# Optimization experiments

Hardware: AMD Instinct MI355X
Metric: run time of the kernel (lower is better)

The kernel has to match this reference:

```python
import jax, jax.numpy as jnp
import numpy as np

B, T, E, H, C = 64, 512, 768, 128, 18


def setup_inputs() -> dict:
    key = jax.random.key(0)
    ks = jax.random.split(key, 16)
    s = 1.0 / np.sqrt(H)
    inp = {
        "x": jax.random.normal(ks[0], (B, T, E), jnp.float32),
        "attention_mask": jnp.ones((B, T), jnp.int32),
        "labels": jax.random.randint(ks[1], (B, T), 0, C, jnp.int32),
        "Wih_f": jax.random.uniform(ks[2], (4 * H, E), jnp.float32, -s, s),
        "Whh_f": jax.random.uniform(ks[3], (4 * H, H), jnp.float32, -s, s),
        "b_f": jax.random.uniform(ks[4], (4 * H,), jnp.float32, -s, s),
        "Wih_b": jax.random.uniform(ks[5], (4 * H, E), jnp.float32, -s, s),
        "Whh_b": jax.random.uniform(ks[6], (4 * H, H), jnp.float32, -s, s),
        "b_b": jax.random.uniform(ks[7], (4 * H,), jnp.float32, -s, s),
        "Wfc": jax.random.uniform(ks[8], (C, 2 * H), jnp.float32, -s, s),
        "bfc": jax.random.uniform(ks[9], (C,), jnp.float32, -s, s),
        "start_trans": jax.random.normal(ks[10], (C,), jnp.float32) * 0.1,
        "end_trans": jax.random.normal(ks[11], (C,), jnp.float32) * 0.1,
        "trans": jax.random.normal(ks[12], (C, C), jnp.float32) * 0.1,
    }
    return inp


def _lstm_dir(x, Wih, Whh, b, reverse=False):
    # x: [B, T, E] -> hidden states [B, T, H]; torch LSTM gate order i,f,g,o
    if reverse:
        x = x[:, ::-1]
    pre = jnp.einsum("bte,ge->btg", x, Wih) + b  # [B, T, 4H] input projection once
    h0 = jnp.zeros((x.shape[0], H), x.dtype)

    def step(carry, pt):
        h, c = carry
        g = pt + h @ Whh.T
        i, f, gg, o = jnp.split(g, 4, axis=-1)
        c = jax.nn.sigmoid(f) * c + jax.nn.sigmoid(i) * jnp.tanh(gg)
        h = jax.nn.sigmoid(o) * jnp.tanh(c)
        return (h, c), h

    _, hs = jax.lax.scan(step, (h0, h0), jnp.swapaxes(pre, 0, 1))
    hs = jnp.swapaxes(hs, 0, 1)
    if reverse:
        hs = hs[:, ::-1]
    return hs


def _crf_loglik(em, tags, mask, start, end, trans):
    # pytorch-crf log-likelihood, batch_first. em [B,T,C], tags/mask [B,T]
    b, t, _ = em.shape
    maskf = mask.astype(em.dtype)
    tags = tags.astype(jnp.int32)
    # numerator: score of the given tag path
    em_sc = jnp.take_along_axis(em, tags[..., None], axis=2)[..., 0]  # [B,T]
    num = start[tags[:, 0]] + em_sc[:, 0]
    num = num + jnp.sum(em_sc[:, 1:] * maskf[:, 1:], axis=1)
    num = num + jnp.sum(trans[tags[:, :-1], tags[:, 1:]] * maskf[:, 1:], axis=1)
    last_idx = jnp.sum(mask.astype(jnp.int32), axis=1) - 1
    last_tags = jnp.take_along_axis(tags, last_idx[:, None], axis=1)[:, 0]
    num = num + end[last_tags]
    # denominator: forward algorithm (logsumexp recurrence over time)
    alpha0 = start + em[:, 0]  # [B,C]

    def step(alpha, inp):
        e_t, m_t = inp
        new = jax.scipy.special.logsumexp(alpha[:, :, None] + trans[None], axis=1) + e_t
        return jnp.where(m_t[:, None], new, alpha), None

    alpha, _ = jax.lax.scan(
        step, alpha0,
        (jnp.swapaxes(em[:, 1:], 0, 1), jnp.swapaxes(mask[:, 1:].astype(bool), 0, 1)),
    )
    den = jax.scipy.special.logsumexp(alpha + end, axis=1)
    return num - den


def _viterbi(em, start, end, trans):
    # em [B,T,C] -> best path [B,T] (full mask)
    s0 = start + em[:, 0]

    def fstep(score, e_t):
        cand = score[:, :, None] + trans[None]  # [B,C,C]
        return jnp.max(cand, axis=1) + e_t, jnp.argmax(cand, axis=1)

    score, bptr = jax.lax.scan(fstep, s0, jnp.swapaxes(em[:, 1:], 0, 1))  # bptr [T-1,B,C]
    last = jnp.argmax(score + end, axis=1)  # [B]

    def bstep(tag, ptr_t):
        prev = jnp.take_along_axis(ptr_t, tag[:, None], axis=1)[:, 0]
        return prev, prev

    _, path = jax.lax.scan(bstep, last, bptr, reverse=True)  # [T-1,B]
    return jnp.concatenate([jnp.swapaxes(path, 0, 1), last[:, None]], axis=1)


def reference(x, attention_mask, labels, Wih_f, Whh_f, b_f, Wih_b, Whh_b, b_b,
              Wfc, bfc, start_trans, end_trans, trans):
    hf = _lstm_dir(x, Wih_f, Whh_f, b_f, reverse=False)
    hb = _lstm_dir(x, Wih_b, Whh_b, b_b, reverse=True)
    seq = jnp.concatenate([hf, hb], axis=-1)  # [B,T,2H]
    em = seq @ Wfc.T + bfc  # [B,T,C] emissions
    mask = attention_mask.astype(bool)
    llh = _crf_loglik(em, labels, mask, start_trans, end_trans, trans)
    loss = -jnp.sum(llh) / x.shape[0]  # reduction='sum' then / batch_size
    path = _viterbi(em, start_trans, end_trans, trans) + 1  # res_paths = x+1
    return path, loss
```

## Files before the change

### kernel.cpp

```cpp
#include <hip/hip_runtime.h>
#include <hip/hip_bf16.h>
#include <math.h>

typedef __attribute__((ext_vector_type(8))) short short8;
typedef __attribute__((ext_vector_type(4))) float f32x4;

constexpr int nB = 64, nT = 512, nE = 768, nH = 128, nG = 512, nC = 18;
constexpr int nBT = nB * nT;

__device__ __forceinline__ float bf2f(unsigned short u) { return __uint_as_float(((unsigned int)u) << 16); }
__device__ __forceinline__ unsigned short f2bf(float f) {
  __hip_bfloat16 h = __float2bfloat16(f);
  return *reinterpret_cast<unsigned short*>(&h);
}
__device__ __forceinline__ float rlane(float v, int lane) {
  return __uint_as_float(__builtin_amdgcn_readlane(__float_as_uint(v), lane));
}
__device__ __forceinline__ float fast_sig(float x) {
  return __builtin_amdgcn_rcpf(1.0f + __builtin_amdgcn_exp2f(-1.44269504f * x));
}
__device__ __forceinline__ float fast_tanh(float x) {
  return 1.0f - 2.0f * __builtin_amdgcn_rcpf(1.0f + __builtin_amdgcn_exp2f(2.88539008f * x));
}
__device__ __forceinline__ float fast_exp(float x) { return __builtin_amdgcn_exp2f(1.44269504f * x); }
__device__ __forceinline__ float fast_log(float x) { return __builtin_amdgcn_logf(x) * 0.69314718f; }

__global__ __launch_bounds__(256) void cvt_kernel(const float* __restrict__ in,
                                                  unsigned short* __restrict__ out, int n8) {
  int i = blockIdx.x * blockDim.x + threadIdx.x;
  const int stride = gridDim.x * blockDim.x;
  for (; i < n8; i += stride) {
    const float4 a = ((const float4*)in)[(size_t)i * 2];
    const float4 b = ((const float4*)in)[(size_t)i * 2 + 1];
    unsigned short u[8] = {f2bf(a.x), f2bf(a.y), f2bf(a.z), f2bf(a.w),
                           f2bf(b.x), f2bf(b.y), f2bf(b.z), f2bf(b.w)};
    ((float4*)out)[i] = *(float4*)u;
  }
}

__global__ __launch_bounds__(256) void proj_kernel(
    const float* __restrict__ x,
    const unsigned short* __restrict__ wfb, const unsigned short* __restrict__ wbb,
    const float* __restrict__ biasF, const float* __restrict__ biasB,
    unsigned short* __restrict__ Pf, unsigned short* __restrict__ Pb)
{
  const int bid = blockIdx.x;
  const int mt = bid & 255, sub = bid >> 8;
  const int dir = sub >> 2, nt = sub & 3;
  const unsigned short* W = dir ? wbb : wfb;
  const float* bias = dir ? biasB : biasF;
  unsigned short* P = dir ? Pb : Pf;
  const int m0 = mt * 128, n0 = nt * 128;

  __shared__ unsigned short As[128 * 40];
  __shared__ unsigned short Bs[128 * 40];
  const int tid = threadIdx.x;
  const int w = tid >> 6, lane = tid & 63, l15 = lane & 15, l4 = lane >> 4;
  const int wr = w >> 1, wc = w & 1;
  const int srow = tid >> 1, shalf = tid & 1;

  const float* srcA = x + (size_t)(m0 + srow) * nE + shalf * 16;
  const unsigned short* srcB = W + (size_t)(n0 + srow) * nE + shalf * 16;

  f32x4 acc[4][4];
#pragma unroll
  for (int i = 0; i < 4; ++i)
#pragma unroll
    for (int j = 0; j < 4; ++j) acc[i][j] = (f32x4){0.f, 0.f, 0.f, 0.f};

  for (int k0 = 0; k0 < nE; k0 += 32) {
    const float4 a0 = *(const float4*)(srcA + k0);
    const float4 a1 = *(const float4*)(srcA + k0 + 4);
    const float4 a2 = *(const float4*)(srcA + k0 + 8);
    const float4 a3 = *(const float4*)(srcA + k0 + 12);
    const float4 b0 = *(const float4*)(srcB + k0);
    const float4 b1 = *(const float4*)(srcB + k0 + 8);
    unsigned short ua[16] = {f2bf(a0.x), f2bf(a0.y), f2bf(a0.z), f2bf(a0.w),
                             f2bf(a1.x), f2bf(a1.y), f2bf(a1.z), f2bf(a1.w),
                             f2bf(a2.x), f2bf(a2.y), f2bf(a2.z), f2bf(a2.w),
                             f2bf(a3.x), f2bf(a3.y), f2bf(a3.z), f2bf(a3.w)};
    __syncthreads();
    *(float4*)&As[srow * 40 + shalf * 16] = *(float4*)&ua[0];
    *(float4*)&As[srow * 40 + shalf * 16 + 8] = *(float4*)&ua[8];
    *(float4*)&Bs[srow * 40 + shalf * 16] = b0;
    *(float4*)&Bs[srow * 40 + shalf * 16 + 8] = b1;
    __syncthreads();
    short8 af[4], bfr[4];
#pragma unroll
    for (int i = 0; i < 4; ++i) af[i] = *(const short8*)&As[(wr * 64 + i * 16 + l15) * 40 + l4 * 8];
#pragma unroll
    for (int j = 0; j < 4; ++j) bfr[j] = *(const short8*)&Bs[(wc * 64 + j * 16 + l15) * 40 + l4 * 8];
#pragma unroll
    for (int i = 0; i < 4; ++i)
#pragma unroll
      for (int j = 0; j < 4; ++j)
        acc[i][j] = __builtin_amdgcn_mfma_f32_16x16x32_bf16(af[i], bfr[j], acc[i][j], 0, 0, 0);
  }
  float bv[4];
#pragma unroll
  for (int j = 0; j < 4; ++j) bv[j] = bias[n0 + wc * 64 + j * 16 + l15];
#pragma unroll
  for (int i = 0; i < 4; ++i) {
#pragma unroll
    for (int j = 0; j < 4; ++j) {
      const int col = n0 + wc * 64 + j * 16 + l15;
#pragma unroll
      for (int r = 0; r < 4; ++r) {
        const int row = m0 + wr * 64 + i * 16 + l4 * 4 + r;
        P[(size_t)row * nG + col] = f2bf(acc[i][j][r] + bv[j]);
      }
    }
  }
}

__global__ __launch_bounds__(512, 1) void lstm_kernel(
    const unsigned short* __restrict__ Pf, const unsigned short* __restrict__ Pb,
    const float* __restrict__ WhhF, const float* __restrict__ WhhB,
    unsigned short* __restrict__ hf, unsigned short* __restrict__ hb)
{
  const int bid = blockIdx.x;
  const int dir = bid & 1, grp = bid >> 1;
  const int b0 = grp * 4;
  const unsigned short* pre = dir ? Pb : Pf;
  const float* Whh = dir ? WhhB : WhhF;
  unsigned short* hout = dir ? hb : hf;

  const int tid = threadIdx.x, w = tid >> 6, lane = tid & 63;
  const int l15 = lane & 15, l4 = lane >> 4;
  const int batch = l15 & 3, msel = l15 >> 2;
  const int cell = w * 16 + msel * 4 + l4;
  const int swz = batch * 40;

  __shared__ unsigned short h_lds[2 * 4 * 128];

  short8 Af[4][4];
#pragma unroll
  for (int m = 0; m < 4; ++m) {
    const int gp = w * 64 + m * 16 + l15;
    const int gorig = (gp & 3) * 128 + (gp >> 2);
#pragma unroll
    for (int kk = 0; kk < 4; ++kk) {
      const float* wp = Whh + (size_t)gorig * nH + kk * 32 + l4 * 8;
      const float4 v0 = *(const float4*)wp;
      const float4 v1 = *(const float4*)(wp + 4);
      unsigned short u[8] = {f2bf(v0.x), f2bf(v0.y), f2bf(v0.z), f2bf(v0.w),
                             f2bf(v1.x), f2bf(v1.y), f2bf(v1.z), f2bf(v1.w)};
      Af[m][kk] = *(short8*)u;
    }
  }
  for (int i = tid; i < 2 * 4 * 128; i += 512) h_lds[i] = 0;

  float c_state = 0.f;
  const unsigned short* pbase = pre + (size_t)(b0 + batch) * nT * nG + cell;

  unsigned short pA[4], pB[4];
  {
    const int tt0 = dir ? (nT - 1) : 0;
    const int tt1 = dir ? (nT - 2) : 1;
#pragma unroll
    for (int r = 0; r < 4; ++r) pA[r] = pbase[(size_t)tt0 * nG + r * 128];
#pragma unroll
    for (int r = 0; r < 4; ++r) pB[r] = pbase[(size_t)tt1 * nG + r * 128];
  }
  __syncthreads();

#define LSTM_STEP(RB, T, BUFC)                                                   \
  {                                                                              \
    const int ttime = dir ? (nT - 1 - (T)) : (T);                                \
    float pg[4];                                                                 \
    _Pragma("unroll")                                                            \
    for (int r = 0; r < 4; ++r) pg[r] = bf2f(BUFC[r]);                           \
    {                                                                            \
      const int tl = ((T) + 2 < nT) ? (T) + 2 : (T);                             \
      const int ttl = dir ? (nT - 1 - tl) : tl;                                  \
      _Pragma("unroll")                                                          \
      for (int r = 0; r < 4; ++r) BUFC[r] = pbase[(size_t)ttl * nG + r * 128];   \
    }                                                                            \
    short8 bfr[4];                                                               \
    _Pragma("unroll")                                                            \
    for (int kk = 0; kk < 4; ++kk) {                                             \
      const int idx = (RB) * 512 + batch * 128 + ((kk * 32 + l4 * 8) ^ swz);     \
      bfr[kk] = *(const short8*)&h_lds[idx];                                     \
    }                                                                            \
    f32x4 acc[4];                                                                \
    _Pragma("unroll")                                                            \
    for (int m = 0; m < 4; ++m) acc[m] = (f32x4){0.f, 0.f, 0.f, 0.f};            \
    _Pragma("unroll")                                                            \
    for (int kk = 0; kk < 4; ++kk)                                               \
      _Pragma("unroll")                                                          \
      for (int m = 0; m < 4; ++m)                                                \
        acc[m] = __builtin_amdgcn_mfma_f32_16x16x32_bf16(Af[m][kk], bfr[kk], acc[m], 0, 0, 0); \
    const float g0 = msel < 2 ? (msel == 0 ? acc[0][0] : acc[1][0]) : (msel == 2 ? acc[2][0] : acc[3][0]); \
    const float g1 = msel < 2 ? (msel == 0 ? acc[0][1] : acc[1][1]) : (msel == 2 ? acc[2][1] : acc[3][1]); \
    const float g2 = msel < 2 ? (msel == 0 ? acc[0][2] : acc[1][2]) : (msel == 2 ? acc[2][2] : acc[3][2]); \
    const float g3 = msel < 2 ? (msel == 0 ? acc[0][3] : acc[1][3]) : (msel == 2 ? acc[2][3] : acc[3][3]); \
    const float gi = g0 + pg[0], gf = g1 + pg[1], gg = g2 + pg[2], go = g3 + pg[3]; \
    c_state = fast_sig(gf) * c_state + fast_sig(gi) * fast_tanh(gg);             \
    const float hval = fast_sig(go) * fast_tanh(c_state);                        \
    const unsigned short hu = f2bf(hval);                                        \
    h_lds[((RB) ^ 1) * 512 + batch * 128 + (cell ^ swz)] = hu;                   \
    hout[((size_t)(b0 + batch) * nT + ttime) * nH + cell] = hu;                  \
    asm volatile("s_waitcnt lgkmcnt(0)" ::: "memory");                           \
    __builtin_amdgcn_sched_barrier(0);                                           \
    __builtin_amdgcn_s_barrier();                                                \
  }

  for (int t2 = 0; t2 < nT; t2 += 2) {
    LSTM_STEP(0, t2, pA)
    LSTM_STEP(1, t2 + 1, pB)
  }
#undef LSTM_STEP
}

__global__ __launch_bounds__(256) void em_kernel(
    const unsigned short* __restrict__ hf, const unsigned short* __restrict__ hb,
    const float* __restrict__ Wfc, const float* __restrict__ bfc,
    float* __restrict__ em)
{
  __shared__ float seq[32][260];
  __shared__ float Wf[18][260];
  const int tid = threadIdx.x;
  const int row0 = blockIdx.x * 32;
  for (int i = tid; i < 32 * 32; i += 256) {
    const int r = i >> 5, seg = i & 31;
    const unsigned short* src = (seg < 16) ? (hf + (size_t)(row0 + r) * nH + seg * 8)
                                           : (hb + (size_t)(row0 + r) * nH + (seg - 16) * 8);
    const float4 v = *(const float4*)src;
    const unsigned short* u = (const unsigned short*)&v;
#pragma unroll
    for (int k = 0; k < 8; ++k) seq[r][seg * 8 + k] = bf2f(u[k]);
  }
  for (int i = tid; i < nC * 256; i += 256) {
    const int cc = i >> 8, k = i & 255;
    Wf[cc][k] = Wfc[cc * 256 + k];
  }
  __syncthreads();
  for (int o = tid; o < 32 * nC; o += 256) {
    const int r = o / nC, cc = o - r * nC;
    float acc = bfc[cc];
    const float4* s4 = (const float4*)&seq[r][0];
    const float4* w4 = (const float4*)&Wf[cc][0];
#pragma unroll
    for (int q = 0; q < 64; ++q) {
      const float4 a = s4[q]; const float4 wv = w4[q];
      acc += a.x * wv.x + a.y * wv.y + a.z * wv.z + a.w * wv.w;
    }
    em[(size_t)(row0 + r) * nC + cc] = acc;
  }
}

__global__ __launch_bounds__(128) void crfvit_kernel(
    const float* __restrict__ em, const int* __restrict__ labels,
    const int* __restrict__ mask, const float* __restrict__ start,
    const float* __restrict__ endt, const float* __restrict__ trans,
    float* __restrict__ llh, float* __restrict__ out_path)
{
  const int b = blockIdx.x; const int tid = threadIdx.x;
  __shared__ float tr[nC * nC];
  __shared__ unsigned char bp[(nT - 1) * nC];
  __shared__ unsigned char path[nT];
  for (int i = tid; i < nC * nC; i += 128) tr[i] = trans[i];
  __syncthreads();
  const float* eb = em + (size_t)b * nT * nC;

#define MAX18(c) fmaxf(fmaxf(fmaxf(fmaxf(fmaxf(c[0], c[1]), c[2]), fmaxf(fmaxf(c[3], c[4]), c[5])),           \
                             fmaxf(fmaxf(fmaxf(c[6], c[7]), c[8]), fmaxf(fmaxf(c[9], c[10]), c[11]))),        \
                       fmaxf(fmaxf(fmaxf(c[12], c[13]), c[14]), fmaxf(fmaxf(c[15], c[16]), c[17])))

  if (tid < 64) {
    const int l = tid;
    const int lc = l < nC ? l : nC - 1;
    const int* tg = labels + (size_t)b * nT;
    const int* mk = mask + (size_t)b * nT;

    float np = 0.f; int cnt = 0;
    for (int t = l; t < nT; t += 64) {
      const int tag = tg[t];
      const float e = eb[(size_t)t * nC + tag];
      if (t == 0) np += start[tag] + e;
      else np += (float)mk[t] * (e + tr[tg[t - 1] * nC + tag]);
      cnt += mk[t];
    }
#pragma unroll
    for (int off = 32; off; off >>= 1) { np += __shfl_xor(np, off); cnt += __shfl_xor(cnt, off); }
    const float num = np + endt[tg[cnt - 1]];

    float trc[nC];
#pragma unroll
    for (int i = 0; i < nC; ++i) trc[i] = tr[i * nC + lc];

    float alpha_r = start[lc] + eb[lc];
    float eA = eb[1 * nC + lc];
    float eB = eb[2 * nC + lc];
    float eC = eb[3 * nC + lc];
    for (int tk = 0; tk < 8; ++tk) {
      const unsigned long long mb = __ballot(mk[tk * 64 + l] != 0);
      for (int tt = (tk == 0 ? 1 : 0); tt < 64; ++tt) {
        const int t = tk * 64 + tt;
        const float ecur = eA; eA = eB; eB = eC;
        const int tl = t + 3 < nT ? t + 3 : nT - 1;
        eC = eb[(size_t)tl * nC + lc];
        float cand[nC];
#pragma unroll
        for (int i = 0; i < nC; ++i) cand[i] = rlane(alpha_r, i) + trc[i];
        const float m = MAX18(cand);
        float ex[nC];
#pragma unroll
        for (int i = 0; i < nC; ++i) ex[i] = fast_exp(cand[i] - m);
        float s = 0.f;
#pragma unroll
        for (int i = 0; i < nC; ++i) s += ex[i];
        const float anew = m + fast_log(s) + ecur;
        alpha_r = ((mb >> tt) & 1) ? anew : alpha_r;
      }
    }
    const float v = (l < nC) ? (alpha_r + endt[l]) : -3.0e38f;
    float m = v;
#pragma unroll
    for (int off = 32; off; off >>= 1) m = fmaxf(m, __shfl_xor(m, off));
    float s = (l < nC) ? fast_exp(v - m) : 0.f;
#pragma unroll
    for (int off = 32; off; off >>= 1) s += __shfl_xor(s, off);
    if (l == 0) llh[b] = num - (m + fast_log(s));
  } else {
    const int l = tid - 64;
    const int lc = l < nC ? l : nC - 1;
    float trc[nC];
#pragma unroll
    for (int i = 0; i < nC; ++i) trc[i] = tr[i * nC + lc];

    float score_r = start[lc] + eb[lc];
    float eA = eb[1 * nC + lc];
    float eB = eb[2 * nC + lc];
    float eC = eb[3 * nC + lc];
    for (int t = 1; t < nT; ++t) {
      const float ecur = eA; eA = eB; eB = eC;
      const int tl = t + 3 < nT ? t + 3 : nT - 1;
      eC = eb[(size_t)tl * nC + lc];
      float cand[nC];
#pragma unroll
      for (int i = 0; i < nC; ++i) cand[i] = rlane(score_r, i) + trc[i];
      const float m = MAX18(cand);
      int sel[nC];
#pragma unroll
      for (int i = 0; i < nC; ++i) sel[i] = (cand[i] == m) ? i : 63;
      int arg = sel[0];
#pragma unroll
      for (int i = 1; i < nC; ++i) arg = min(arg, sel[i]);
      score_r = m + ecur;
      if (l < nC) bp[(t - 1) * nC + l] = (unsigned char)arg;
    }
    if (l == 0) {
      float mm = -3.0e38f; int last = 0;
      for (int i = 0; i < nC; ++i) {
        const float v = rlane(score_r, i) + endt[i];
        if (v > mm) { mm = v; last = i; }
      }
      path[nT - 1] = (unsigned char)last;
      int cur = last;
      for (int t = nT - 2; t >= 0; --t) { cur = bp[t * nC + cur]; path[t] = (unsigned char)cur; }
    }
    asm volatile("s_waitcnt lgkmcnt(0)" ::: "memory");
    __builtin_amdgcn_wave_barrier();
    for (int t = l; t < nT; t += 64) out_path[(size_t)b * nT + t] = (float)(path[t] + 1);
  }
#undef MAX18
}

__global__ __launch_bounds__(64) void loss_kernel(const float* __restrict__ llh, float* __restrict__ out)
{
  const int l = threadIdx.x;
  float v = llh[l];
#pragma unroll
  for (int off = 32; off; off >>= 1) v += __shfl_xor(v, off);
  if (l == 0) out[0] = -v / (float)nB;
}

extern "C" void kernel_launch(void* const* d_in, const int* in_sizes, int n_in,
                              void* d_out, int out_size, void* d_ws, size_t ws_size,
                              hipStream_t stream)
{
  const float* x      = (const float*)d_in[0];
  const int*   amask  = (const int*)d_in[1];
  const int*   labels = (const int*)d_in[2];
  const float* Wih_f  = (const float*)d_in[3];
  const float* Whh_f  = (const float*)d_in[4];
  const float* b_f    = (const float*)d_in[5];
  const float* Wih_b  = (const float*)d_in[6];
  const float* Whh_b  = (const float*)d_in[7];
  const float* b_b    = (const float*)d_in[8];
  const float* Wfc    = (const float*)d_in[9];
  const float* bfc    = (const float*)d_in[10];
  const float* start  = (const float*)d_in[11];
  const float* endt   = (const float*)d_in[12];
  const float* trans  = (const float*)d_in[13];

  float* out = (float*)d_out;
  float* ws = (float*)d_ws;
  unsigned short* preF = (unsigned short*)ws;
  unsigned short* preB = preF + (size_t)nBT * nG;
  unsigned short* hf   = preB + (size_t)nBT * nG;
  unsigned short* hb   = hf + (size_t)nBT * nH;
  float* em  = (float*)(hb + (size_t)nBT * nH);
  float* llh = em + (size_t)nBT * nC;
  unsigned short* wfb = (unsigned short*)(llh + 64);
  unsigned short* wbb = wfb + (size_t)nG * nE;

  cvt_kernel<<<192, 256, 0, stream>>>(Wih_f, wfb, nG * nE / 8);
  cvt_kernel<<<192, 256, 0, stream>>>(Wih_b, wbb, nG * nE / 8);
  proj_kernel<<<2048, 256, 0, stream>>>(x, wfb, wbb, b_f, b_b, preF, preB);
  lstm_kernel<<<32, 512, 0, stream>>>(preF, preB, Whh_f, Whh_b, hf, hb);
  em_kernel<<<1024, 256, 0, stream>>>(hf, hb, Wfc, bfc, em);
  crfvit_kernel<<<64, 128, 0, stream>>>(em, labels, amask, start, endt, trans, llh, out);
  loss_kernel<<<1, 64, 0, stream>>>(llh, out + nBT);
}
```

Before: 549.0 us.

## Fuse input projection and LSTM into one kernel with per-quarter flag handoff

Merges the input-projection GEMM and the recurrent LSTM into one persistent launch. The first 32 blocks run the recurrence while the remaining blocks compute projection tiles, ordered by time quarter and direction, and signal completion through atomic flags. LSTM blocks spin-wait on a quarter's flags before consuming it, so the sequential recurrence overlaps with the projection work. This relies on the LSTM blocks being co-resident with the producer blocks. It adds flag memsets and spin-wait overhead, and the projection tile is reshaped to 128x256 with 512 threads.

```diff
diff --git a/kernel.cpp b/kernel.cpp
--- a/kernel.cpp
+++ b/kernel.cpp
@@ -7,6 +7,7 @@
 
 constexpr int nB = 64, nT = 512, nE = 768, nH = 128, nG = 512, nC = 18;
 constexpr int nBT = nB * nT;
+constexpr int N_LSTM_BLK = 32, N_PROJ_BLK = 1024;
 
 __device__ __forceinline__ float bf2f(unsigned short u) { return __uint_as_float(((unsigned int)u) << 16); }
 __device__ __forceinline__ unsigned short f2bf(float f) {
@@ -38,86 +39,95 @@
   }
 }
 
-__global__ __launch_bounds__(256) void proj_kernel(
+__global__ __launch_bounds__(512, 2) void fused_kernel(
     const float* __restrict__ x,
     const unsigned short* __restrict__ wfb, const unsigned short* __restrict__ wbb,
     const float* __restrict__ biasF, const float* __restrict__ biasB,
-    unsigned short* __restrict__ Pf, unsigned short* __restrict__ Pb)
+    unsigned short* __restrict__ Pf, unsigned short* __restrict__ Pb,
+    const float* __restrict__ WhhF, const float* __restrict__ WhhB,
+    unsigned short* __restrict__ hf, unsigned short* __restrict__ hb,
+    int* __restrict__ flags)
 {
-  const int bid = blockIdx.x;
-  const int mt = bid & 255, sub = bid >> 8;
-  const int dir = sub >> 2, nt = sub & 3;
-  const unsigned short* W = dir ? wbb : wfb;
-  const float* bias = dir ? biasB : biasF;
-  unsigned short* P = dir ? Pb : Pf;
-  const int m0 = mt * 128, n0 = nt * 128;
-
-  __shared__ unsigned short As[128 * 40];
-  __shared__ unsigned short Bs[128 * 40];
+  __shared__ __align__(16) unsigned short smem[15360];
   const int tid = threadIdx.x;
-  const int w = tid >> 6, lane = tid & 63, l15 = lane & 15, l4 = lane >> 4;
-  const int wr = w >> 1, wc = w & 1;
-  const int srow = tid >> 1, shalf = tid & 1;
-
-  const float* srcA = x + (size_t)(m0 + srow) * nE + shalf * 16;
-  const unsigned short* srcB = W + (size_t)(n0 + srow) * nE + shalf * 16;
-
-  f32x4 acc[4][4];
-#pragma unroll
-  for (int i = 0; i < 4; ++i)
-#pragma unroll
-    for (int j = 0; j < 4; ++j) acc[i][j] = (f32x4){0.f, 0.f, 0.f, 0.f};
-
-  for (int k0 = 0; k0 < nE; k0 += 32) {
-    const float4 a0 = *(const float4*)(srcA + k0);
-    const float4 a1 = *(const float4*)(srcA + k0 + 4);
-    const float4 a2 = *(const float4*)(srcA + k0 + 8);
-    const float4 a3 = *(const float4*)(srcA + k0 + 12);
-    const float4 b0 = *(const float4*)(srcB + k0);
-    const float4 b1 = *(const float4*)(srcB + k0 + 8);
-    unsigned short ua[16] = {f2bf(a0.x), f2bf(a0.y), f2bf(a0.z), f2bf(a0.w),
-                             f2bf(a1.x), f2bf(a1.y), f2bf(a1.z), f2bf(a1.w),
-                             f2bf(a2.x), f2bf(a2.y), f2bf(a2.z), f2bf(a2.w),
-                             f2bf(a3.x), f2bf(a3.y), f2bf(a3.z), f2bf(a3.w)};
+
+  if (blockIdx.x >= N_LSTM_BLK) {
+    const int p = blockIdx.x - N_LSTM_BLK;
+    const int round = p >> 8;
+    const int r = p & 255;
+    const int dir = r & 1;
+    const int rem = r >> 1;
+    const int b = rem >> 1;
+    const int snt = rem & 1;
+    const int tq = dir ? (3 - round) : round;
+    const unsigned short* W = dir ? wbb : wfb;
+    const float* bias = dir ? biasB : biasF;
+    unsigned short* P = dir ? Pb : Pf;
+    const int m0 = b * nT + tq * 128;
+    const int n0 = snt * 256;
+
+    unsigned short* As = smem;
+    unsigned short* Bs = smem + 5120;
+
+    const int w = tid >> 6, lane = tid & 63, l15 = lane & 15, l4 = lane >> 4;
+    const int wr = w >> 2, wc = w & 3;
+    const int arow = tid >> 2, aq = tid & 3;
+    const int brow = tid >> 1, bh = tid & 1;
+
+    const float* srcA = x + (size_t)(m0 + arow) * nE + aq * 8;
+    const unsigned short* srcB = W + (size_t)(n0 + brow) * nE + bh * 16;
+
+    f32x4 acc[4][4];
+#pragma unroll
+    for (int i = 0; i < 4; ++i)
+#pragma unroll
+      for (int j = 0; j < 4; ++j) acc[i][j] = (f32x4){0.f, 0.f, 0.f, 0.f};
+
+    for (int k0 = 0; k0 < nE; k0 += 32) {
+      const float4 a0 = *(const float4*)(srcA + k0);
+      const float4 a1 = *(const float4*)(srcA + k0 + 4);
+      const float4 b0 = *(const float4*)(srcB + k0);
+      const float4 b1 = *(const float4*)(srcB + k0 + 8);
+      unsigned short ua[8] = {f2bf(a0.x), f2bf(a0.y), f2bf(a0.z), f2bf(a0.w),
+                              f2bf(a1.x), f2bf(a1.y), f2bf(a1.z), f2bf(a1.w)};
+      __syncthreads();
+      *(float4*)&As[arow * 40 + aq * 8] = *(float4*)ua;
+      *(float4*)&Bs[brow * 40 + bh * 16] = b0;
+      *(float4*)&Bs[brow * 40 + bh * 16 + 8] = b1;
+      __syncthreads();
+      short8 af[4], bfr[4];
+#pragma unroll
+      for (int i = 0; i < 4; ++i) af[i] = *(const short8*)&As[(wr * 64 + i * 16 + l15) * 40 + l4 * 8];
+#pragma unroll
+      for (int j = 0; j < 4; ++j) bfr[j] = *(const short8*)&Bs[(wc * 64 + j * 16 + l15) * 40 + l4 * 8];
+#pragma unroll
+      for (int i = 0; i < 4; ++i)
+#pragma unroll
+        for (int j = 0; j < 4; ++j)
+          acc[i][j] = __builtin_amdgcn_mfma_f32_16x16x32_bf16(af[i], bfr[j], acc[i][j], 0, 0, 0);
+    }
+    float bv[4];
+#pragma unroll
+    for (int j = 0; j < 4; ++j) bv[j] = bias[n0 + wc * 64 + j * 16 + l15];
+#pragma unroll
+    for (int i = 0; i < 4; ++i) {
+#pragma unroll
+      for (int j = 0; j < 4; ++j) {
+        const int col = n0 + wc * 64 + j * 16 + l15;
+#pragma unroll
+        for (int rr = 0; rr < 4; ++rr) {
+          const int row = m0 + wr * 64 + i * 16 + l4 * 4 + rr;
+          P[(size_t)row * nG + col] = f2bf(acc[i][j][rr] + bv[j]);
+        }
+      }
+    }
     __syncthreads();
-    *(float4*)&As[srow * 40 + shalf * 16] = *(float4*)&ua[0];
-    *(float4*)&As[srow * 40 + shalf * 16 + 8] = *(float4*)&ua[8];
-    *(float4*)&Bs[srow * 40 + shalf * 16] = b0;
-    *(float4*)&Bs[srow * 40 + shalf * 16 + 8] = b1;
-    __syncthreads();
-    short8 af[4], bfr[4];
-#pragma unroll
-    for (int i = 0; i < 4; ++i) af[i] = *(const short8*)&As[(wr * 64 + i * 16 + l15) * 40 + l4 * 8];
-#pragma unroll
-    for (int j = 0; j < 4; ++j) bfr[j] = *(const short8*)&Bs[(wc * 64 + j * 16 + l15) * 40 + l4 * 8];
-#pragma unroll
-    for (int i = 0; i < 4; ++i)
-#pragma unroll
-      for (int j = 0; j < 4; ++j)
-        acc[i][j] = __builtin_amdgcn_mfma_f32_16x16x32_bf16(af[i], bfr[j], acc[i][j], 0, 0, 0);
-  }
-  float bv[4];
-#pragma unroll
-  for (int j = 0; j < 4; ++j) bv[j] = bias[n0 + wc * 64 + j * 16 + l15];
-#pragma unroll
-  for (int i = 0; i < 4; ++i) {
-#pragma unroll
-    for (int j = 0; j < 4; ++j) {
-      const int col = n0 + wc * 64 + j * 16 + l15;
-#pragma unroll
-      for (int r = 0; r < 4; ++r) {
-        const int row = m0 + wr * 64 + i * 16 + l4 * 4 + r;
-        P[(size_t)row * nG + col] = f2bf(acc[i][j][r] + bv[j]);
-      }
-    }
-  }
-}
-
-__global__ __launch_bounds__(512, 1) void lstm_kernel(
-    const unsigned short* __restrict__ Pf, const unsigned short* __restrict__ Pb,
-    const float* __restrict__ WhhF, const float* __restrict__ WhhB,
-    unsigned short* __restrict__ hf, unsigned short* __restrict__ hb)
-{
+    if (tid == 0)
+      __hip_atomic_fetch_add(&flags[(dir * 64 + b) * 4 + tq], 1,
+                             __ATOMIC_RELEASE, __HIP_MEMORY_SCOPE_AGENT);
+    return;
+  }
+
   const int bid = blockIdx.x;
   const int dir = bid & 1, grp = bid >> 1;
   const int b0 = grp * 4;
@@ -125,13 +135,13 @@
   const float* Whh = dir ? WhhB : WhhF;
   unsigned short* hout = dir ? hb : hf;
 
-  const int tid = threadIdx.x, w = tid >> 6, lane = tid & 63;
+  const int w = tid >> 6, lane = tid & 63;
   const int l15 = lane & 15, l4 = lane >> 4;
   const int batch = l15 & 3, msel = l15 >> 2;
   const int cell = w * 16 + msel * 4 + l4;
   const int swz = batch * 40;
 
-  __shared__ unsigned short h_lds[2 * 4 * 128];
+  unsigned short* h_lds = smem;
 
   short8 Af[4][4];
 #pragma unroll
@@ -149,6 +159,19 @@
     }
   }
   for (int i = tid; i < 2 * 4 * 128; i += 512) h_lds[i] = 0;
+  __syncthreads();
+
+#define WAIT_QUARTER(QL)                                                         \
+  {                                                                              \
+    const int tq_ = dir ? (3 - (QL)) : (QL);                                     \
+    for (int bq_ = 0; bq_ < 4; ++bq_) {                                          \
+      while (__hip_atomic_load(&flags[(dir * 64 + b0 + bq_) * 4 + tq_],          \
+                               __ATOMIC_ACQUIRE, __HIP_MEMORY_SCOPE_AGENT) < 2)  \
+        __builtin_amdgcn_s_sleep(8);                                             \
+    }                                                                            \
+  }
+
+  WAIT_QUARTER(0)
 
   float c_state = 0.f;
   const unsigned short* pbase = pre + (size_t)(b0 + batch) * nT * nG + cell;
@@ -162,7 +185,6 @@
 #pragma unroll
     for (int r = 0; r < 4; ++r) pB[r] = pbase[(size_t)tt1 * nG + r * 128];
   }
-  __syncthreads();
 
 #define LSTM_STEP(RB, T, BUFC)                                                   \
   {                                                                              \
@@ -206,10 +228,12 @@
   }
 
   for (int t2 = 0; t2 < nT; t2 += 2) {
+    if ((t2 & 127) == 126 && t2 + 2 < nT) WAIT_QUARTER((t2 + 2) >> 7)
     LSTM_STEP(0, t2, pA)
     LSTM_STEP(1, t2 + 1, pB)
   }
 #undef LSTM_STEP
+#undef WAIT_QUARTER
 }
 
 __global__ __launch_bounds__(256) void em_kernel(
@@ -405,11 +429,13 @@
   float* llh = em + (size_t)nBT * nC;
   unsigned short* wfb = (unsigned short*)(llh + 64);
   unsigned short* wbb = wfb + (size_t)nG * nE;
-
+  int* flags = (int*)(wbb + (size_t)nG * nE);
+
+  hipMemsetAsync(flags, 0, 512 * sizeof(int), stream);
   cvt_kernel<<<192, 256, 0, stream>>>(Wih_f, wfb, nG * nE / 8);
   cvt_kernel<<<192, 256, 0, stream>>>(Wih_b, wbb, nG * nE / 8);
-  proj_kernel<<<2048, 256, 0, stream>>>(x, wfb, wbb, b_f, b_b, preF, preB);
-  lstm_kernel<<<32, 512, 0, stream>>>(preF, preB, Whh_f, Whh_b, hf, hb);
+  fused_kernel<<<N_LSTM_BLK + N_PROJ_BLK, 512, 0, stream>>>(
+      x, wfb, wbb, b_f, b_b, preF, preB, Whh_f, Whh_b, hf, hb, flags);
   em_kernel<<<1024, 256, 0, stream>>>(hf, hb, Wfc, bfc, em);
   crfvit_kernel<<<64, 128, 0, stream>>>(em, labels, amask, start, endt, trans, llh, out);
   loss_kernel<<<1, 64, 0, stream>>>(llh, out + nBT);
```

Measured after the change: 587.3 us. +7.0%, slower.
